# Kernel optimization log

Hardware: AMD Instinct MI355X
Metric: run time of the kernel (lower is better)

Reference implementation:

```python
import jax, jax.numpy as jnp
import numpy as np

BN_EPS = 1e-5

def _l2norm(x):
    n = jnp.sqrt(jnp.sum(x * x, axis=-1, keepdims=True))
    return x / jnp.maximum(n, 1e-12)

def _bn_eval(x, gamma, beta):
    # eval-mode BatchNorm2d (running_mean=0, running_var=1)
    g = gamma / jnp.sqrt(1.0 + BN_EPS)
    return x * g[None, :, None, None] + beta[None, :, None, None]

def _forward(feat, Wq, Wk, Wv, ad_conv_w, ad_conv_b, pm_w1, pm_w2,
             back_w, catt, catt1, mlp_w, mlp_b, mlp_gamma, mlp_beta,
             dsn_w, dsn_b, dsn_gamma, dsn_beta):
    B, C, H, W = feat.shape
    p = pm_w1.shape[1]  # p_num (top-k size)
    x2d = feat.reshape(B, C, H * W).transpose(0, 2, 1)          # [B,HW,C]
    q = jnp.einsum('bnc,dc->bnd', x2d, Wq)                       # [B,HW,cim]
    k = jnp.einsum('bnc,dc->bnd', x2d, Wk)
    v = jnp.einsum('bnc,dc->bnd', x2d, Wv)
    # cosine-similarity attention weights [B,HW,HW]
    w = jnp.einsum('bid,bjd->bij', _l2norm(q), _l2norm(k))
    wv, idx = jax.lax.top_k(w, p)                                # [B,HW,p]
    vg = jax.vmap(lambda vv, ii: vv[ii])(v, idx)                 # [B,HW,p,cim] gather
    # ADConv: 1x1 conv on a single channel == scalar affine
    xa = wv * ad_conv_w[0] + ad_conv_b[0]
    pos = jnp.where(xa > 0, xa, 0.0)
    hdn = jax.nn.relu(jnp.einsum('bip,qp->biq', pos, pm_w1))     # [B,HW,2p]
    mask = jax.nn.sigmoid(jnp.einsum('biq,pq->bip', hdn, pm_w2)) # [B,HW,p]
    att = jax.nn.softmax(jnp.where(xa > 0, xa, -100000.0), axis=-1)
    wfin = att * mask                                            # [B,HW,p]
    ov = jnp.einsum('bip,bipd->bid', wfin, vg)                   # [B,HW,cim]
    ov = jnp.einsum('bid,cd->bic', ov, back_w)                   # [B,HW,C]
    v_img = catt * ov.transpose(0, 2, 1).reshape(B, C, H, W)
    cat = jnp.concatenate([v_img, catt1 * feat], axis=1)         # [B,2C,H,W]
    x = jnp.einsum('oc,bchw->bohw', mlp_w, cat) + mlp_b[None, :, None, None]
    x = jax.nn.relu(_bn_eval(x, mlp_gamma, mlp_beta))
    r0 = jnp.einsum('oc,bchw->bohw', dsn_w, x) + dsn_b[None, :, None, None]
    r0 = jax.nn.relu(_bn_eval(r0, dsn_gamma, dsn_beta))
    return x, r0

def setup_inputs() -> dict:
    key = jax.random.key(0)
    ks = jax.random.split(key, 12)
    B, C, H, W = 2, 256, 80, 80
    cim, p = C // 8, 9
    sc = 0.05
    return {
        'feat': jax.random.normal(ks[0], (B, C, H, W), jnp.float32),
        'Wq': jax.random.normal(ks[1], (cim, C), jnp.float32) * sc,
        'Wk': jax.random.normal(ks[2], (cim, C), jnp.float32) * sc,
        'Wv': jax.random.normal(ks[3], (cim, C), jnp.float32) * sc,
        'ad_conv_w': jnp.ones((1,), jnp.float32),
        'ad_conv_b': jnp.zeros((1,), jnp.float32),
        'pm_w1': jax.random.normal(ks[4], (2 * p, p), jnp.float32) * 0.3,
        'pm_w2': jax.random.normal(ks[5], (p, 2 * p), jnp.float32) * 0.3,
        'back_w': jax.random.normal(ks[6], (C, cim), jnp.float32) * sc,
        'catt': jnp.ones((1, C, 1, 1), jnp.float32),
        'catt1': jnp.ones((1, C, 1, 1), jnp.float32),
        'mlp_w': jax.random.normal(ks[7], (C, 2 * C), jnp.float32) * sc,
        'mlp_b': jnp.zeros((C,), jnp.float32),
        'mlp_gamma': jnp.ones((C,), jnp.float32),
        'mlp_beta': jnp.zeros((C,), jnp.float32),
        'dsn_w': jax.random.normal(ks[8], (1, C), jnp.float32) * sc,
        'dsn_b': jnp.zeros((1,), jnp.float32),
        'dsn_gamma': jnp.ones((1,), jnp.float32),
        'dsn_beta': jnp.zeros((1,), jnp.float32),
        'H': H,
        'W': W,
    }

def reference(feat, Wq, Wk, Wv, ad_conv_w, ad_conv_b, pm_w1, pm_w2,
              back_w, catt, catt1, mlp_w, mlp_b, mlp_gamma, mlp_beta,
              dsn_w, dsn_b, dsn_gamma, dsn_beta, H, W):
    # H,W < 768 -> get_forward branch
    return _forward(feat, Wq, Wk, Wv, ad_conv_w, ad_conv_b, pm_w1, pm_w2,
                    back_w, catt, catt1, mlp_w, mlp_b, mlp_gamma, mlp_beta,
                    dsn_w, dsn_b, dsn_gamma, dsn_beta)
```

## Files before the change

### kernel.cpp

```cpp
#include <hip/hip_runtime.h>
#include <hip/hip_bf16.h>

#define HW   6400
#define NB   2
#define CC   256
#define CIM  32
#define PP   9
#define P2   18
#define ROWS (NB*HW)
#define NCH  32
#define JCH  (HW/NCH)
#define NGRP (ROWS/64)

typedef float f4 __attribute__((ext_vector_type(4)));

#define OFF_QN   0
#define OFF_KN   (OFF_QN + ROWS*CIM)
#define OFF_V    (OFF_KN + ROWS*CIM)
#define OFF_OV   (OFF_V  + ROWS*CIM)
#define OFF_PV   (OFF_OV + ROWS*CIM)
#define OFF_PI   (OFF_PV + ROWS*NCH*PP)
#define OFF_W1T  (OFF_PI + ROWS*NCH*PP)
#define OFF_W2T  (OFF_W1T + CIM*CC)
#define OFF_BF   (OFF_W2T + CC*CC)
#define OFF_WQT  (OFF_BF + CC)
#define OFF_WKT  (OFF_WQT + CC*CIM)
#define OFF_WVT  (OFF_WKT + CC*CIM)

__global__ void prep_kernel(const float* __restrict__ mlp_w, const float* __restrict__ mlp_b,
                            const float* __restrict__ mlp_g, const float* __restrict__ mlp_be,
                            const float* __restrict__ back_w, const float* __restrict__ catt,
                            const float* __restrict__ catt1,
                            const float* __restrict__ Wq, const float* __restrict__ Wk,
                            const float* __restrict__ Wv, float* __restrict__ ws) {
    const int blk = blockIdx.x, t = threadIdx.x;
    const float bnc = rsqrtf(1.0f + 1e-5f);
    if (blk < 32) {
        const int d = blk, o = t;
        const float g = mlp_g[o] * bnc;
        float acc = 0.f;
        for (int c = 0; c < CC; ++c)
            acc = fmaf(mlp_w[o*512 + c] * catt[c], back_w[c*CIM + d], acc);
        ws[OFF_W1T + d*CC + o] = g * acc;
    } else if (blk == 32) {
        const int o = t;
        const float g = mlp_g[o] * bnc;
        for (int c = 0; c < CC; ++c)
            ws[OFF_W2T + c*CC + o] = g * mlp_w[o*512 + 256 + c] * catt1[c];
        ws[OFF_BF + o] = g * mlp_b[o] + mlp_be[o];
    } else {
        const float* W = (blk == 33) ? Wq : (blk == 34) ? Wk : Wv;
        float* WT = ws + ((blk == 33) ? OFF_WQT : (blk == 34) ? OFF_WKT : OFF_WVT);
        for (int i = t; i < CC*CIM; i += 256) {
            const int c = i / CIM, d = i % CIM;
            WT[c*CIM + d] = W[d*CC + c];
        }
    }
}

__global__ __launch_bounds__(256) void qkv_kernel(const float* __restrict__ feat,
                                                  const float* __restrict__ ws_r,
                                                  float* __restrict__ ws) {
    __shared__ float part[4][64][33];
    __shared__ float invA[64];
    const int bx = blockIdx.x;
    const int mat = bx % 3;
    const int ng  = bx / 3;
    const int n0  = ng * 64;
    const int b   = n0 / HW;
    const int nsp0 = n0 % HW;
    const int tid = threadIdx.x;
    const int w = __builtin_amdgcn_readfirstlane(tid >> 6);
    const int lane = tid & 63;
    const float* WT = ws_r + (mat == 0 ? OFF_WQT : mat == 1 ? OFF_WKT : OFF_WVT);
    const float* fbase = feat + (size_t)b*CC*HW + nsp0 + lane;
    float acc[CIM];
#pragma unroll
    for (int d = 0; d < CIM; ++d) acc[d] = 0.f;
    const int c0 = w * 64;
    for (int cc = 0; cc < 64; ++cc) {
        const int c = c0 + cc;
        const float fv = fbase[(size_t)c * HW];
        const float* wt = WT + c*CIM;
#pragma unroll
        for (int d = 0; d < CIM; ++d) acc[d] = fmaf(fv, wt[d], acc[d]);
    }
#pragma unroll
    for (int d = 0; d < CIM; ++d) part[w][lane][d] = acc[d];
    __syncthreads();
    {
        const int n = tid >> 2, d0 = (tid & 3) * 8;
#pragma unroll
        for (int dd = 0; dd < 8; ++dd) {
            const int d = d0 + dd;
            part[0][n][d] = part[0][n][d] + part[1][n][d] + part[2][n][d] + part[3][n][d];
        }
    }
    __syncthreads();
    if (mat < 2) {
        if (tid < 64) {
            const int n = tid;
            float ss = 0.f;
#pragma unroll
            for (int d = 0; d < CIM; ++d) { const float x = part[0][n][d]; ss = fmaf(x, x, ss); }
            invA[n] = 1.0f / fmaxf(sqrtf(ss), 1e-12f);
        }
        __syncthreads();
    }
    float* outp = ws + (mat == 0 ? OFF_QN : mat == 1 ? OFF_KN : OFF_V);
    {
        const int n = tid >> 2, d0 = (tid & 3) * 8;
        const float scl = (mat < 2) ? invA[n] : 1.0f;
        const size_t r = (size_t)(n0 + n);
#pragma unroll
        for (int dd = 0; dd < 8; ++dd)
            outp[r*CIM + d0 + dd] = part[0][n][d0 + dd] * scl;
    }
}

__global__ __launch_bounds__(256, 3) void attn_kernel(const float* __restrict__ ws_r,
                                                      float* __restrict__ ws) {
    const int tid  = threadIdx.x;
    const int wid  = (blockIdx.x << 2) + (tid >> 6);
    const int lane = tid & 63;
    const int rg = __builtin_amdgcn_readfirstlane(wid >> 5);
    const int ch = __builtin_amdgcn_readfirstlane(wid & (NCH-1));
    const int r = rg*64 + lane;
    const int b = (rg*64) / HW;
    const float* qn = ws_r + OFF_QN + (size_t)r*CIM;
    float q[CIM];
    {   const f4* qv = (const f4*)qn;
        f4* q4 = (f4*)q;
#pragma unroll
        for (int h = 0; h < 8; ++h) q4[h] = qv[h];
    }
    const float* kbase = ws_r + OFF_KN + ((size_t)b*HW + ch*JCH)*CIM;
    const int jbase = ch*JCH;
    float tv[PP]; int ti[PP];
#pragma unroll
    for (int s = 0; s < PP; ++s) { tv[s] = -3.0e38f; ti[s] = 0; }
#pragma unroll 2
    for (int j = 0; j < JCH; ++j) {
        const float* kp = kbase + j*CIM;
        float a0 = 0.f, a1 = 0.f, a2 = 0.f, a3 = 0.f;
#pragma unroll
        for (int d = 0; d < CIM; d += 4) {
            a0 = fmaf(q[d+0], kp[d+0], a0);
            a1 = fmaf(q[d+1], kp[d+1], a1);
            a2 = fmaf(q[d+2], kp[d+2], a2);
            a3 = fmaf(q[d+3], kp[d+3], a3);
        }
        const float wv = (a0 + a1) + (a2 + a3);
        if (wv > tv[8]) {
            tv[8] = wv; ti[8] = jbase + j;
#pragma unroll
            for (int s = 8; s > 0; --s) {
                const bool sw = tv[s] > tv[s-1];
                const float vA = tv[s-1], vB = tv[s];
                tv[s-1] = sw ? vB : vA;  tv[s] = sw ? vA : vB;
                const int iA = ti[s-1], iB = ti[s];
                ti[s-1] = sw ? iB : iA;  ti[s] = sw ? iA : iB;
            }
        }
    }
    float* pv = ws + OFF_PV + ((size_t)r*NCH + ch)*PP;
    int*   pi = (int*)(ws + OFF_PI) + ((size_t)r*NCH + ch)*PP;
#pragma unroll
    for (int s = 0; s < PP; ++s) { pv[s] = tv[s]; pi[s] = ti[s]; }
}

#define NSLOT 5
__global__ __launch_bounds__(256) void merge_kernel(const float* __restrict__ ws_r,
                                                    const float* __restrict__ pm_w1,
                                                    const float* __restrict__ pm_w2,
                                                    const float* __restrict__ ad_w,
                                                    const float* __restrict__ ad_b,
                                                    float* __restrict__ ws) {
    __shared__ float pm1[P2*PP];
    __shared__ float pm2[PP*P2];
    const int tid = threadIdx.x;
    for (int i = tid; i < P2*PP; i += 256) pm1[i] = pm_w1[i];
    for (int i = tid; i < PP*P2; i += 256) pm2[i] = pm_w2[i];
    __syncthreads();
    const int w = tid >> 6, lane = tid & 63;
    const int r = blockIdx.x*4 + w;
    const int b = r / HW;
    const float* pv = ws_r + OFF_PV + (size_t)r*NCH*PP;
    const int*   pi = (const int*)(ws_r + OFF_PI) + (size_t)r*NCH*PP;
    float cv[NSLOT]; int ci[NSLOT];
#pragma unroll
    for (int i = 0; i < NSLOT; ++i) {
        const int s = lane + 64*i;
        if (s < NCH*PP) { cv[i] = pv[s]; ci[i] = pi[s]; }
        else            { cv[i] = -3e38f; ci[i] = 0x7fffffff; }
    }
    float topv[PP]; int topi[PP];
#pragma unroll
    for (int rd = 0; rd < PP; ++rd) {
        float hv = cv[0]; int hi = ci[0]; int hs = 0;
#pragma unroll
        for (int i = 1; i < NSLOT; ++i)
            if (cv[i] > hv || (cv[i] == hv && ci[i] < hi)) { hv = cv[i]; hi = ci[i]; hs = i; }
        float bv = hv; int bi = hi;
#pragma unroll
        for (int off = 32; off >= 1; off >>= 1) {
            const float ov_ = __shfl_xor(bv, off);
            const int   oi_ = __shfl_xor(bi, off);
            if (ov_ > bv || (ov_ == bv && oi_ < bi)) { bv = ov_; bi = oi_; }
        }
        const bool won = (hv == bv && hi == bi);
#pragma unroll
        for (int i = 0; i < NSLOT; ++i)
            if (won && i == hs) cv[i] = -3e38f;
        topv[rd] = bv;
        topi[rd] = (bi >= 0 && bi < HW) ? bi : 0;
    }
    const float adw = ad_w[0], adb = ad_b[0];
    float xa[PP], pos[PP];
#pragma unroll
    for (int p = 0; p < PP; ++p) { xa[p] = fmaf(topv[p], adw, adb); pos[p] = fmaxf(xa[p], 0.f); }
    float hdn[P2];
#pragma unroll
    for (int qq = 0; qq < P2; ++qq) {
        float a = 0.f;
#pragma unroll
        for (int p = 0; p < PP; ++p) a = fmaf(pos[p], pm1[qq*PP + p], a);
        hdn[qq] = fmaxf(a, 0.f);
    }
    float msk[PP];
#pragma unroll
    for (int p = 0; p < PP; ++p) {
        float a = 0.f;
#pragma unroll
        for (int qq = 0; qq < P2; ++qq) a = fmaf(hdn[qq], pm2[p*P2 + qq], a);
        msk[p] = 1.0f / (1.0f + expf(-a));
    }
    float xm[PP], m = -3e38f;
#pragma unroll
    for (int p = 0; p < PP; ++p) { xm[p] = xa[p] > 0.f ? xa[p] : -100000.0f; m = fmaxf(m, xm[p]); }
    float e[PP], ssum = 0.f;
#pragma unroll
    for (int p = 0; p < PP; ++p) { e[p] = expf(xm[p] - m); ssum += e[p]; }
    float wf[PP];
#pragma unroll
    for (int p = 0; p < PP; ++p) wf[p] = (e[p] / ssum) * msk[p];
    const int d = lane & 31;
    const float* vb = ws_r + OFF_V + (size_t)b*HW*CIM;
    float acc = 0.f;
#pragma unroll
    for (int p = 0; p < PP; ++p) acc = fmaf(wf[p], vb[(size_t)topi[p]*CIM + d], acc);
    if (lane < 32) ws[OFF_OV + (size_t)r*CIM + d] = acc;
}

__global__ __launch_bounds__(64) void fin_kernel(const float* __restrict__ feat,
                                                 const float* __restrict__ ws_r,
                                                 float* __restrict__ out) {
    __shared__ float ovt[64*33];
    const int bx = blockIdx.x;
    const int ng = bx % NGRP;
    const int og = bx / NGRP;
    const int n0 = ng*64;
    const int b  = n0 / HW;
    const int nsp0 = n0 % HW;
    const int lane = threadIdx.x;
    const float4* ovg = (const float4*)(ws_r + OFF_OV + (size_t)n0*CIM);
#pragma unroll
    for (int i = 0; i < 8; ++i) {
        const int f = lane + 64*i;
        const float4 vv = ovg[f];
        const int row = f >> 3, col = (f & 7) * 4;
        ovt[row*33 + col]     = vv.x;
        ovt[row*33 + col + 1] = vv.y;
        ovt[row*33 + col + 2] = vv.z;
        ovt[row*33 + col + 3] = vv.w;
    }
    __syncthreads();
    const int o0 = og * 16;
    float acc[16];
    const float* bfp = ws_r + OFF_BF;
#pragma unroll
    for (int oi = 0; oi < 16; ++oi) acc[oi] = bfp[o0 + oi];
    const float* w1t = ws_r + OFF_W1T;
#pragma unroll 4
    for (int dd = 0; dd < CIM; ++dd) {
        const float xv = ovt[lane*33 + dd];
        const float* wrow = w1t + dd*CC + o0;
#pragma unroll
        for (int oi = 0; oi < 16; ++oi) acc[oi] = fmaf(xv, wrow[oi], acc[oi]);
    }
    const float* w2t = ws_r + OFF_W2T;
    const float* fbase = feat + (size_t)b*CC*HW + nsp0 + lane;
#pragma unroll 4
    for (int c = 0; c < CC; ++c) {
        const float fv = fbase[(size_t)c * HW];
        const float* wrow = w2t + c*CC + o0;
#pragma unroll
        for (int oi = 0; oi < 16; ++oi) acc[oi] = fmaf(fv, wrow[oi], acc[oi]);
    }
    const size_t obase = (size_t)b*CC*HW + nsp0 + lane;
#pragma unroll
    for (int oi = 0; oi < 16; ++oi)
        out[obase + (size_t)(o0 + oi)*HW] = fmaxf(acc[oi], 0.f);
}

__global__ __launch_bounds__(256) void dsn_kernel(const float* __restrict__ xout,
                                                  const float* __restrict__ dsn_w,
                                                  const float* __restrict__ dsn_b,
                                                  const float* __restrict__ dsn_g,
                                                  const float* __restrict__ dsn_be,
                                                  float* __restrict__ out) {
    const int t = blockIdx.x*256 + threadIdx.x;
    const int b = t / HW, nsp = t % HW;
    const float* xb = xout + (size_t)b*CC*HW + nsp;
    float acc = 0.f;
#pragma unroll 4
    for (int o = 0; o < CC; ++o)
        acc = fmaf(xb[(size_t)o*HW], dsn_w[o], acc);
    const float g = dsn_g[0] * rsqrtf(1.0f + 1e-5f);
    const float r0 = fmaxf(fmaf(g, acc + dsn_b[0], dsn_be[0]), 0.f);
    out[(size_t)NB*CC*HW + t] = r0;
}

extern "C" void kernel_launch(void* const* d_in, const int* in_sizes, int n_in,
                              void* d_out, int out_size, void* d_ws, size_t ws_size,
                              hipStream_t stream) {
    const float* feat  = (const float*)d_in[0];
    const float* Wq    = (const float*)d_in[1];
    const float* Wk    = (const float*)d_in[2];
    const float* Wv    = (const float*)d_in[3];
    const float* adw   = (const float*)d_in[4];
    const float* adb   = (const float*)d_in[5];
    const float* pm_w1 = (const float*)d_in[6];
    const float* pm_w2 = (const float*)d_in[7];
    const float* backw = (const float*)d_in[8];
    const float* catt  = (const float*)d_in[9];
    const float* catt1 = (const float*)d_in[10];
    const float* mlp_w = (const float*)d_in[11];
    const float* mlp_b = (const float*)d_in[12];
    const float* mlp_g = (const float*)d_in[13];
    const float* mlp_be= (const float*)d_in[14];
    const float* dsn_w = (const float*)d_in[15];
    const float* dsn_b = (const float*)d_in[16];
    const float* dsn_g = (const float*)d_in[17];
    const float* dsn_be= (const float*)d_in[18];
    float* ws = (float*)d_ws;
    float* out = (float*)d_out;

    prep_kernel<<<36, 256, 0, stream>>>(mlp_w, mlp_b, mlp_g, mlp_be, backw, catt, catt1,
                                        Wq, Wk, Wv, ws);
    qkv_kernel<<<NGRP*3, 256, 0, stream>>>(feat, ws, ws);
    attn_kernel<<<(NGRP*NCH)/4, 256, 0, stream>>>(ws, ws);
    merge_kernel<<<ROWS/4, 256, 0, stream>>>(ws, pm_w1, pm_w2, adw, adb, ws);
    fin_kernel<<<NGRP*16, 64, 0, stream>>>(feat, ws, out);
    dsn_kernel<<<ROWS/256, 256, 0, stream>>>(out, dsn_w, dsn_b, dsn_g, dsn_be, out);
}
```

Before: 362.6 us.

## Replace per-chunk top-k sort with sampled threshold and atomic candidate filtering

Top-k selection becomes a two-pass scheme. A sampling pass scores every 8th key to find a lower bound on each row's 9th-largest value. A second full pass computes all scores and appends only those at or above that threshold to a capped per-row buffer using atomics, and the final merge reduces over those few candidates. This removes the per-element insertion sort from the inner loop. In exchange it adds an extra strided pass, two kernels, global atomics, and a cap of 256 candidates per row that could drop valid entries (with tie-ordering changes) if too many scores pass the threshold.

```diff
diff --git a/kernel.cpp b/kernel.cpp
--- a/kernel.cpp
+++ b/kernel.cpp
@@ -11,6 +11,7 @@
 #define NCH  32
 #define JCH  (HW/NCH)
 #define NGRP (ROWS/64)
+#define CAPR 256
 
 typedef float f4 __attribute__((ext_vector_type(4)));
 
@@ -26,6 +27,9 @@
 #define OFF_WQT  (OFF_BF + CC)
 #define OFF_WKT  (OFF_WQT + CC*CIM)
 #define OFF_WVT  (OFF_WKT + CC*CIM)
+#define OFF_TH   (OFF_WVT + CC*CIM)
+#define OFF_SC   (OFF_TH + ROWS)
+#define OFF_SV   OFF_PV
 
 __global__ void prep_kernel(const float* __restrict__ mlp_w, const float* __restrict__ mlp_b,
                             const float* __restrict__ mlp_g, const float* __restrict__ mlp_be,
@@ -118,8 +122,8 @@
     }
 }
 
-__global__ __launch_bounds__(256, 3) void attn_kernel(const float* __restrict__ ws_r,
-                                                      float* __restrict__ ws) {
+__global__ __launch_bounds__(256) void attn_sample(const float* __restrict__ ws_r,
+                                                   float* __restrict__ ws) {
     const int tid  = threadIdx.x;
     const int wid  = (blockIdx.x << 2) + (tid >> 6);
     const int lane = tid & 63;
@@ -139,8 +143,7 @@
     float tv[PP]; int ti[PP];
 #pragma unroll
     for (int s = 0; s < PP; ++s) { tv[s] = -3.0e38f; ti[s] = 0; }
-#pragma unroll 2
-    for (int j = 0; j < JCH; ++j) {
+    for (int j = 0; j < JCH; j += 8) {
         const float* kp = kbase + j*CIM;
         float a0 = 0.f, a1 = 0.f, a2 = 0.f, a3 = 0.f;
 #pragma unroll
@@ -170,12 +173,98 @@
 }
 
 #define NSLOT 5
-__global__ __launch_bounds__(256) void merge_kernel(const float* __restrict__ ws_r,
-                                                    const float* __restrict__ pm_w1,
-                                                    const float* __restrict__ pm_w2,
-                                                    const float* __restrict__ ad_w,
-                                                    const float* __restrict__ ad_b,
+__global__ __launch_bounds__(256) void theta_kernel(const float* __restrict__ ws_r,
                                                     float* __restrict__ ws) {
+    const int tid = threadIdx.x;
+    const int w = tid >> 6, lane = tid & 63;
+    const int r = blockIdx.x*4 + w;
+    const float* pv = ws_r + OFF_PV + (size_t)r*NCH*PP;
+    const int*   pi = (const int*)(ws_r + OFF_PI) + (size_t)r*NCH*PP;
+    float cv[NSLOT]; int ci[NSLOT];
+#pragma unroll
+    for (int i = 0; i < NSLOT; ++i) {
+        const int s = lane + 64*i;
+        if (s < NCH*PP) { cv[i] = pv[s]; ci[i] = pi[s]; }
+        else            { cv[i] = -3e38f; ci[i] = 0x7fffffff; }
+    }
+    float s9 = -3e38f;
+#pragma unroll
+    for (int rd = 0; rd < PP; ++rd) {
+        float hv = cv[0]; int hi = ci[0]; int hs = 0;
+#pragma unroll
+        for (int i = 1; i < NSLOT; ++i)
+            if (cv[i] > hv || (cv[i] == hv && ci[i] < hi)) { hv = cv[i]; hi = ci[i]; hs = i; }
+        float bv = hv; int bi = hi;
+#pragma unroll
+        for (int off = 32; off >= 1; off >>= 1) {
+            const float ov_ = __shfl_xor(bv, off);
+            const int   oi_ = __shfl_xor(bi, off);
+            if (ov_ > bv || (ov_ == bv && oi_ < bi)) { bv = ov_; bi = oi_; }
+        }
+        const bool won = (hv == bv && hi == bi);
+#pragma unroll
+        for (int i = 0; i < NSLOT; ++i)
+            if (won && i == hs) cv[i] = -3e38f;
+        s9 = bv;
+    }
+    if (lane == 0) {
+        ws[OFF_TH + r] = s9;
+        ((int*)(ws + OFF_SC))[r] = 0;
+    }
+}
+
+__global__ __launch_bounds__(256) void attn_filter(const float* __restrict__ ws_r,
+                                                   float* __restrict__ ws) {
+    const int tid  = threadIdx.x;
+    const int wid  = (blockIdx.x << 2) + (tid >> 6);
+    const int lane = tid & 63;
+    const int rg = __builtin_amdgcn_readfirstlane(wid >> 5);
+    const int ch = __builtin_amdgcn_readfirstlane(wid & (NCH-1));
+    const int r = rg*64 + lane;
+    const int b = (rg*64) / HW;
+    const float* qn = ws_r + OFF_QN + (size_t)r*CIM;
+    float q[CIM];
+    {   const f4* qv = (const f4*)qn;
+        f4* q4 = (f4*)q;
+#pragma unroll
+        for (int h = 0; h < 8; ++h) q4[h] = qv[h];
+    }
+    const float th = ws_r[OFF_TH + r];
+    int* sc = (int*)(ws + OFF_SC);
+    float* sv = ws + OFF_SV;
+    const float* kbase = ws_r + OFF_KN + ((size_t)b*HW + ch*JCH)*CIM;
+    const int jbase = ch*JCH;
+#pragma unroll 2
+    for (int j = 0; j < JCH; ++j) {
+        const float* kp = kbase + j*CIM;
+        float a0 = 0.f, a1 = 0.f, a2 = 0.f, a3 = 0.f;
+#pragma unroll
+        for (int d = 0; d < CIM; d += 4) {
+            a0 = fmaf(q[d+0], kp[d+0], a0);
+            a1 = fmaf(q[d+1], kp[d+1], a1);
+            a2 = fmaf(q[d+2], kp[d+2], a2);
+            a3 = fmaf(q[d+3], kp[d+3], a3);
+        }
+        const float wv = (a0 + a1) + (a2 + a3);
+        if (wv >= th) {
+            const int slot = atomicAdd(&sc[r], 1);
+            if (slot < CAPR) {
+                float2 pr;
+                pr.x = wv;
+                pr.y = __int_as_float(jbase + j);
+                *(float2*)(sv + ((size_t)r*CAPR + slot)*2) = pr;
+            }
+        }
+    }
+}
+
+#define NS2 4
+__global__ __launch_bounds__(256) void merge2_kernel(const float* __restrict__ ws_r,
+                                                     const float* __restrict__ pm_w1,
+                                                     const float* __restrict__ pm_w2,
+                                                     const float* __restrict__ ad_w,
+                                                     const float* __restrict__ ad_b,
+                                                     float* __restrict__ ws) {
     __shared__ float pm1[P2*PP];
     __shared__ float pm2[PP*P2];
     const int tid = threadIdx.x;
@@ -185,21 +274,24 @@
     const int w = tid >> 6, lane = tid & 63;
     const int r = blockIdx.x*4 + w;
     const int b = r / HW;
-    const float* pv = ws_r + OFF_PV + (size_t)r*NCH*PP;
-    const int*   pi = (const int*)(ws_r + OFF_PI) + (size_t)r*NCH*PP;
-    float cv[NSLOT]; int ci[NSLOT];
-#pragma unroll
-    for (int i = 0; i < NSLOT; ++i) {
+    const int cnt0 = ((const int*)(ws_r + OFF_SC))[r];
+    const int cnl = cnt0 < CAPR ? cnt0 : CAPR;
+    const float* svp = ws_r + OFF_SV + (size_t)r*CAPR*2;
+    float cv[NS2]; int ci[NS2];
+#pragma unroll
+    for (int i = 0; i < NS2; ++i) {
         const int s = lane + 64*i;
-        if (s < NCH*PP) { cv[i] = pv[s]; ci[i] = pi[s]; }
-        else            { cv[i] = -3e38f; ci[i] = 0x7fffffff; }
+        if (s < cnl) {
+            const float2 pr = *(const float2*)(svp + (size_t)s*2);
+            cv[i] = pr.x; ci[i] = __float_as_int(pr.y);
+        } else { cv[i] = -3e38f; ci[i] = 0x7fffffff; }
     }
     float topv[PP]; int topi[PP];
 #pragma unroll
     for (int rd = 0; rd < PP; ++rd) {
         float hv = cv[0]; int hi = ci[0]; int hs = 0;
 #pragma unroll
-        for (int i = 1; i < NSLOT; ++i)
+        for (int i = 1; i < NS2; ++i)
             if (cv[i] > hv || (cv[i] == hv && ci[i] < hi)) { hv = cv[i]; hi = ci[i]; hs = i; }
         float bv = hv; int bi = hi;
 #pragma unroll
@@ -210,7 +302,7 @@
         }
         const bool won = (hv == bv && hi == bi);
 #pragma unroll
-        for (int i = 0; i < NSLOT; ++i)
+        for (int i = 0; i < NS2; ++i)
             if (won && i == hs) cv[i] = -3e38f;
         topv[rd] = bv;
         topi[rd] = (bi >= 0 && bi < HW) ? bi : 0;
@@ -349,8 +441,10 @@
     prep_kernel<<<36, 256, 0, stream>>>(mlp_w, mlp_b, mlp_g, mlp_be, backw, catt, catt1,
                                         Wq, Wk, Wv, ws);
     qkv_kernel<<<NGRP*3, 256, 0, stream>>>(feat, ws, ws);
-    attn_kernel<<<(NGRP*NCH)/4, 256, 0, stream>>>(ws, ws);
-    merge_kernel<<<ROWS/4, 256, 0, stream>>>(ws, pm_w1, pm_w2, adw, adb, ws);
+    attn_sample<<<(NGRP*NCH)/4, 256, 0, stream>>>(ws, ws);
+    theta_kernel<<<ROWS/4, 256, 0, stream>>>(ws, ws);
+    attn_filter<<<(NGRP*NCH)/4, 256, 0, stream>>>(ws, ws);
+    merge2_kernel<<<ROWS/4, 256, 0, stream>>>(ws, pm_w1, pm_w2, adw, adb, ws);
     fin_kernel<<<NGRP*16, 64, 0, stream>>>(feat, ws, out);
     dsn_kernel<<<ROWS/256, 256, 0, stream>>>(out, dsn_w, dsn_b, dsn_g, dsn_be, out);
 }
```

After: 313.4 us. -13.6%, faster.
